# Optimization experiments

Hardware: AMD Instinct MI355X
Metric: run time of the kernel (lower is better)

The kernel has to match this reference:

```python
import jax, jax.numpy as jnp
import numpy as np
from jax import lax

B, S, H, T = 64, 512, 1024, 24


def setup_inputs() -> dict:
    key = jax.random.key(0)
    k1, k2, k3, k4, k5 = jax.random.split(key, 5)
    feats = jax.random.normal(k1, (B, S, H), dtype=jnp.float32)
    target = jax.random.randint(k2, (B, S), 0, T)  # tag ids (argmax of original one-hot target)
    # descending-sorted lengths -> prefix mask, matching the torch code's sorted-batch assumption
    lengths = jnp.sort(jax.random.randint(k3, (B,), S // 2, S + 1))[::-1]
    mask = jnp.arange(S)[None, :] < lengths[:, None]  # (B,S) bool
    # hidden2tag params (uniform init ~ nn.Linear default scale)
    bound = 1.0 / np.sqrt(H)
    W = jax.random.uniform(k4, (T, H), minval=-bound, maxval=bound, dtype=jnp.float32)
    b = jax.random.uniform(k5, (T,), minval=-bound, maxval=bound, dtype=jnp.float32)
    transition = jnp.zeros((T, T), dtype=jnp.float32)
    return {"feats": feats, "target": target, "mask": mask, "W": W, "b": b, "transition": transition}


def reference(feats, target, mask, W, b, transition):
    # emission scores: (B,S,T)
    emission = jnp.einsum("bsh,th->bst", feats, W) + b
    # gold path score
    sc = jnp.take_along_axis(emission, target[:, :, None], axis=2).squeeze(-1)  # (B,S)
    sc = sc.at[:, 1:].add(transition[target[:, :-1], target[:, 1:]])
    total_score = (sc * mask.astype(emission.dtype)).sum(axis=1)  # (B,)
    # forward algorithm (log-partition) as a scan over time
    p0 = emission[:, 0]  # (B,T)
    emis_t = jnp.swapaxes(emission[:, 1:], 0, 1)  # (S-1,B,T)
    mask_t = jnp.swapaxes(mask[:, 1:], 0, 1)      # (S-1,B)

    def step(p, xs):
        emit_i, m_i = xs
        # log_sum[b, prev, cur] = p[b, prev] + transition[prev, cur] + emit_i[b, cur]
        new_p = jax.nn.logsumexp(p[:, :, None] + transition[None, :, :] + emit_i[:, None, :], axis=1)
        return jnp.where(m_i[:, None], new_p, p), None

    p, _ = lax.scan(step, p0, (emis_t, mask_t))
    log_Z = jax.nn.logsumexp(p, axis=1)  # (B,)
    loss = -jnp.mean(total_score - log_Z)
    return loss, emission
```

## Files before the change

### kernel.cpp

```cpp
#include <hip/hip_runtime.h>
#include <cstdint>
#include <math.h>

#define B_ 64
#define S_ 512
#define H_ 1024
#define T_ 24
#define TP_ 32
#define NC_ 32
#define CL_ 16
#define KST_ 1040

typedef unsigned int u32;
typedef unsigned short u16;
typedef __attribute__((ext_vector_type(8))) short short8v;
typedef __attribute__((ext_vector_type(4))) float f32x4;
typedef __attribute__((ext_vector_type(4))) u32 uint4v;

__device__ __forceinline__ float rl_f32(float x, int sl) {
    return __uint_as_float(__builtin_amdgcn_readlane(__float_as_uint(x), sl));
}

__device__ __forceinline__ void split_pk(float f0, float f1, u32& hpk, u32& lpk) {
    const u32 u0 = __float_as_uint(f0), u1 = __float_as_uint(f1);
    const u32 t1 = u1 & 0xffff0000u;
    hpk = (u0 >> 16) | t1;
    const float fl0 = f0 - __uint_as_float(u0 & 0xffff0000u);
    const float fl1 = f1 - __uint_as_float(t1);
    lpk = (__float_as_uint(fl0) >> 16) | (__float_as_uint(fl1) & 0xffff0000u);
}

__global__ __launch_bounds__(256) void wcvt_kernel(const float* __restrict__ W,
                                                   u16* __restrict__ Wh,
                                                   u16* __restrict__ Wl,
                                                   float* __restrict__ out) {
    const int i = blockIdx.x * 256 + threadIdx.x;
    if (i == 0) out[0] = 0.f;
    const int t = i >> 10;
    const float f = (t < T_) ? W[i] : 0.f;
    const u32 u = __float_as_uint(f);
    const u32 rh = u + 0x7fffu + ((u >> 16) & 1u);
    const u16 hb = (u16)(rh >> 16);
    const float fh = __uint_as_float((u32)hb << 16);
    const float fl = f - fh;
    const u32 u2 = __float_as_uint(fl);
    const u32 rl2 = u2 + 0x7fffu + ((u2 >> 16) & 1u);
    Wh[i] = hb;
    Wl[i] = (u16)(rl2 >> 16);
}

__global__ __launch_bounds__(256, 4) void gemm_kernel(const float* __restrict__ feats,
                                                      const u16* __restrict__ Wh,
                                                      const u16* __restrict__ Wl,
                                                      const float* __restrict__ bias,
                                                      float* __restrict__ emission) {
    __shared__ f32x4 ldsP[2][64][2];
    const int tid  = threadIdx.x;
    const int lane = tid & 63;
    const int wv   = tid >> 6;
    const int mt_in = wv & 1;
    const int kh    = wv >> 1;
    const int r16  = lane & 15;
    const int g    = lane >> 4;
    const int mtile = blockIdx.x * 2 + mt_in;

    const long ko0 = (long)kh * 512 + g * 8;
    const float* ap  = feats + ((long)mtile * 16 + r16) * H_ + ko0;
    const u16* bh0p = Wh + r16 * H_ + ko0;
    const u16* bl0p = Wl + r16 * H_ + ko0;
    const u16* bh1p = Wh + (r16 + 16) * H_ + ko0;
    const u16* bl1p = Wl + (r16 + 16) * H_ + ko0;

    f32x4 acc0 = {0.f, 0.f, 0.f, 0.f};
    f32x4 acc1 = {0.f, 0.f, 0.f, 0.f};

    float4 A0[3], A1[3];
    short8v BH0[3], BL0[3], BH1[3], BL1[3];
#pragma unroll
    for (int p = 0; p < 3; ++p) {
        const int ko = p * 32;
        A0[p]  = *(const float4*)(ap + ko);
        A1[p]  = *(const float4*)(ap + ko + 4);
        BH0[p] = *(const short8v*)(bh0p + ko);
        BL0[p] = *(const short8v*)(bl0p + ko);
        BH1[p] = *(const short8v*)(bh1p + ko);
        BL1[p] = *(const short8v*)(bl1p + ko);
    }

#pragma unroll
    for (int kk = 0; kk < 16; ++kk) {
        const int sl = kk % 3;
        const float4 a0 = A0[sl];
        const float4 a1 = A1[sl];
        const short8v bh0 = BH0[sl];
        const short8v bl0 = BL0[sl];
        const short8v bh1 = BH1[sl];
        const short8v bl1 = BL1[sl];
        if (kk + 3 < 16) {
            const int ko = (kk + 3) * 32;
            A0[sl]  = *(const float4*)(ap + ko);
            A1[sl]  = *(const float4*)(ap + ko + 4);
            BH0[sl] = *(const short8v*)(bh0p + ko);
            BL0[sl] = *(const short8v*)(bl0p + ko);
            BH1[sl] = *(const short8v*)(bh1p + ko);
            BL1[sl] = *(const short8v*)(bl1p + ko);
        }

        u32 h0, l0, h1, l1, h2, l2, h3, l3;
        split_pk(a0.x, a0.y, h0, l0);
        split_pk(a0.z, a0.w, h1, l1);
        split_pk(a1.x, a1.y, h2, l2);
        split_pk(a1.z, a1.w, h3, l3);
        const uint4v hv = {h0, h1, h2, h3};
        const uint4v lv = {l0, l1, l2, l3};
        const short8v ah = __builtin_bit_cast(short8v, hv);
        const short8v al = __builtin_bit_cast(short8v, lv);

        acc0 = __builtin_amdgcn_mfma_f32_16x16x32_bf16(al, bh0, acc0, 0, 0, 0);
        acc0 = __builtin_amdgcn_mfma_f32_16x16x32_bf16(ah, bl0, acc0, 0, 0, 0);
        acc0 = __builtin_amdgcn_mfma_f32_16x16x32_bf16(ah, bh0, acc0, 0, 0, 0);
        acc1 = __builtin_amdgcn_mfma_f32_16x16x32_bf16(al, bh1, acc1, 0, 0, 0);
        acc1 = __builtin_amdgcn_mfma_f32_16x16x32_bf16(ah, bl1, acc1, 0, 0, 0);
        acc1 = __builtin_amdgcn_mfma_f32_16x16x32_bf16(ah, bh1, acc1, 0, 0, 0);
    }

    if (kh == 1) {
        ldsP[mt_in][lane][0] = acc0;
        ldsP[mt_in][lane][1] = acc1;
    }
    __syncthreads();
    if (kh == 0) {
        const f32x4 p0 = ldsP[mt_in][lane][0];
        const f32x4 p1 = ldsP[mt_in][lane][1];
#pragma unroll
        for (int r = 0; r < 4; ++r) {
            acc0[r] += p0[r];
            acc1[r] += p1[r];
        }
        const float b0 = bias[r16];
        const float b1 = (r16 + 16 < T_) ? bias[r16 + 16] : 0.f;
        float* op = emission + ((long)mtile * 16 + g * 4) * T_;
#pragma unroll
        for (int r = 0; r < 4; ++r) {
            op[r * T_ + r16] = acc0[r] + b0;
            if (r16 + 16 < T_) op[r * T_ + r16 + 16] = acc1[r] + b1;
        }
    }
}

__global__ __launch_bounds__(64, 1) void chunk_kernel(const float* __restrict__ emission,
                                                      const int* __restrict__ mask,
                                                      const float* __restrict__ trans,
                                                      float* __restrict__ wsK) {
    __shared__ u32 lds[2][2][16][18];
    const int bid = blockIdx.x;
    const int c_ = bid & (NC_ - 1);
    const int b  = bid >> 5;
    const int l  = threadIdx.x;
    const int cc = l & 15;
    const int q  = l >> 4;
    const int aq4 = (l & 48);

    const float* em = emission + (long)b * S_ * T_;
    const int* mk = mask + b * S_;

    int mc = 0;
#pragma unroll
    for (int k = 0; k < 8; ++k) mc += mk[l + k * 64];
#pragma unroll
    for (int off = 32; off; off >>= 1) mc += __shfl_xor(mc, off);
    const int len = __builtin_amdgcn_readfirstlane(mc);

    const int lo = 1 + c_ * CL_;
    const int hi = min(lo + CL_, S_);
    const int send = min(hi, len);

    short8v Ah[2], Al[2];
#pragma unroll
    for (int I = 0; I < 2; ++I) {
        const int j = 16 * I + cc;
        u32 hw[4], lw[4];
#pragma unroll
        for (int w = 0; w < 4; ++w) {
            const int t0 = 8 * q + 2 * w;
            const float v0 = (t0 < 24 && j < 24) ? __expf(trans[t0 * T_ + j]) : 0.f;
            const float v1 = (t0 + 1 < 24 && j < 24) ? __expf(trans[(t0 + 1) * T_ + j]) : 0.f;
            split_pk(v0, v1, hw[w], lw[w]);
        }
        const uint4v hv = {hw[0], hw[1], hw[2], hw[3]};
        const uint4v lv = {lw[0], lw[1], lw[2], lw[3]};
        Ah[I] = __builtin_bit_cast(short8v, hv);
        Al[I] = __builtin_bit_cast(short8v, lv);
    }

    f32x4 K[2][2];
#pragma unroll
    for (int I = 0; I < 2; ++I)
#pragma unroll
        for (int J = 0; J < 2; ++J)
#pragma unroll
            for (int r = 0; r < 4; ++r)
                K[I][J][r] = (16 * I + 4 * q + r == 16 * J + cc) ? 1.f : 0.f;

    u32 bh[2][4], bl[2][4];
#pragma unroll
    for (int J = 0; J < 2; ++J)
#pragma unroll
        for (int w = 0; w < 4; ++w) {
            const int k0 = 8 * q + 2 * w, col = 16 * J + cc;
            bh[J][w] = (k0 == col ? 0x3f80u : 0u) | (k0 + 1 == col ? 0x3f800000u : 0u);
            bl[J][w] = 0u;
        }

    const int xj = ((l & 31) < 24) ? (l & 31) : 0;
    float xr_[CL_];
#pragma unroll
    for (int k = 0; k < CL_; ++k) {
        const int s = lo + k;
        xr_[k] = em[((s < S_) ? s : 0) * T_ + xj];
    }

    float Ls = 0.f;
    const f32x4 z4 = {0.f, 0.f, 0.f, 0.f};

#pragma unroll
    for (int k = 0; k < CL_; ++k) {
        const int s = lo + k;
        if (s < send) {
            const uint4v bh0v = {bh[0][0], bh[0][1], bh[0][2], bh[0][3]};
            const uint4v bh1v = {bh[1][0], bh[1][1], bh[1][2], bh[1][3]};
            const uint4v bl0v = {bl[0][0], bl[0][1], bl[0][2], bl[0][3]};
            const uint4v bl1v = {bl[1][0], bl[1][1], bl[1][2], bl[1][3]};
            const short8v B0h = __builtin_bit_cast(short8v, bh0v);
            const short8v B1h = __builtin_bit_cast(short8v, bh1v);
            const short8v B0l = __builtin_bit_cast(short8v, bl0v);
            const short8v B1l = __builtin_bit_cast(short8v, bl1v);

            f32x4 acc[2][2];
#pragma unroll
            for (int I = 0; I < 2; ++I) {
                acc[I][0] = __builtin_amdgcn_mfma_f32_16x16x32_bf16(Ah[I], B0h, z4, 0, 0, 0);
                acc[I][0] = __builtin_amdgcn_mfma_f32_16x16x32_bf16(Ah[I], B0l, acc[I][0], 0, 0, 0);
                acc[I][0] = __builtin_amdgcn_mfma_f32_16x16x32_bf16(Al[I], B0h, acc[I][0], 0, 0, 0);
                acc[I][1] = __builtin_amdgcn_mfma_f32_16x16x32_bf16(Ah[I], B1h, z4, 0, 0, 0);
                acc[I][1] = __builtin_amdgcn_mfma_f32_16x16x32_bf16(Ah[I], B1l, acc[I][1], 0, 0, 0);
                acc[I][1] = __builtin_amdgcn_mfma_f32_16x16x32_bf16(Al[I], B1h, acc[I][1], 0, 0, 0);
            }

            const float X = __expf(xr_[k]);
            const int xi = __float_as_int(X);
            float xr0[4], xr1[4];
#pragma unroll
            for (int r = 0; r < 4; ++r) {
                xr0[r] = __int_as_float(__builtin_amdgcn_ds_bpermute(aq4 + 4 * r, xi));
                xr1[r] = __int_as_float(__builtin_amdgcn_ds_bpermute(aq4 + 64 + 4 * r, xi));
            }
#pragma unroll
            for (int J = 0; J < 2; ++J)
#pragma unroll
                for (int r = 0; r < 4; ++r) {
                    K[0][J][r] = acc[0][J][r] * xr0[r];
                    K[1][J][r] = acc[1][J][r] * xr1[r];
                }

            if (k == 7 || k == CL_ - 1) {
                float mx = K[0][0][0];
#pragma unroll
                for (int I = 0; I < 2; ++I)
#pragma unroll
                    for (int J = 0; J < 2; ++J)
#pragma unroll
                        for (int r = 0; r < 4; ++r) mx = fmaxf(mx, K[I][J][r]);
#pragma unroll
                for (int off = 32; off; off >>= 1) mx = fmaxf(mx, __shfl_xor(mx, off));
                const u32 ef = __float_as_uint(mx) & 0x7f800000u;
                const float inv = __uint_as_float(0x7f000000u - ef);
#pragma unroll
                for (int I = 0; I < 2; ++I)
#pragma unroll
                    for (int J = 0; J < 2; ++J)
#pragma unroll
                        for (int r = 0; r < 4; ++r) K[I][J][r] *= inv;
                Ls += (float)((int)(ef >> 23) - 127) * 0.6931471805599453f;
            }

            if (k < CL_ - 1) {
#pragma unroll
                for (int I = 0; I < 2; ++I)
#pragma unroll
                    for (int J = 0; J < 2; ++J)
#pragma unroll
                        for (int m = 0; m < 2; ++m) {
                            u32 h, lo_w;
                            split_pk(K[I][J][2 * m], K[I][J][2 * m + 1], h, lo_w);
                            const int p = 8 * I + 2 * q + m;
                            lds[0][J][p][cc] = h;
                            lds[1][J][p][cc] = lo_w;
                        }
#pragma unroll
                for (int J = 0; J < 2; ++J)
#pragma unroll
                    for (int w = 0; w < 4; ++w) {
                        bh[J][w] = lds[0][J][4 * q + w][cc];
                        bl[J][w] = lds[1][J][4 * q + w][cc];
                    }
            }
        }
    }

    float* outp = wsK + (long)(b * NC_ + c_) * KST_;
#pragma unroll
    for (int I = 0; I < 2; ++I)
#pragma unroll
        for (int J = 0; J < 2; ++J)
#pragma unroll
            for (int r = 0; r < 4; ++r)
                outp[(16 * I + 4 * q + r) * 32 + 16 * J + cc] = K[I][J][r];
    if (l == 0) outp[1024] = Ls;
}

#define ACC4(kv, t0)                                                           \
    s0 = fmaf(rl_f32(p, (t0) + 0), kv.x, s0);                                  \
    s1 = fmaf(rl_f32(p, (t0) + 1), kv.y, s1);                                  \
    s2 = fmaf(rl_f32(p, (t0) + 2), kv.z, s2);                                  \
    s3 = fmaf(rl_f32(p, (t0) + 3), kv.w, s3);

__global__ __launch_bounds__(64) void finalize_kernel(const float* __restrict__ emission,
                                                      const int* __restrict__ target,
                                                      const int* __restrict__ mask,
                                                      const float* __restrict__ trans,
                                                      const float* __restrict__ wsK,
                                                      float* __restrict__ out) {
    const int b = blockIdx.x;
    const int j = threadIdx.x;
    const int jj = j < 24 ? j : 23;
    const float* em = emission + (long)b * S_ * T_;
    const int* mk = mask + b * S_;

    float p = (j < 24) ? __expf(em[j]) : 0.f;
    float C = 0.f;

    for (int c = 0; c < NC_; ++c) {
        const float* base = wsK + (long)(b * NC_ + c) * KST_;
        C += base[1024];
        const float4* rp = (const float4*)(base + jj * 32);
        const float4 k0 = rp[0], k1 = rp[1], k2 = rp[2], k3 = rp[3], k4 = rp[4], k5 = rp[5];
        float s0 = 0.f, s1 = 0.f, s2 = 0.f, s3 = 0.f;
        ACC4(k0, 0) ACC4(k1, 4) ACC4(k2, 8) ACC4(k3, 12) ACC4(k4, 16) ACC4(k5, 20)
        p = (j < 24) ? ((s0 + s1) + (s2 + s3)) : 0.f;
        float mx = p;
#pragma unroll
        for (int off = 32; off; off >>= 1) mx = fmaxf(mx, __shfl_xor(mx, off));
        const u32 ef = __float_as_uint(mx) & 0x7f800000u;
        p *= __uint_as_float(0x7f000000u - ef);
        C += (float)((int)(ef >> 23) - 127) * 0.6931471805599453f;
    }

    float ex = p;
#pragma unroll
    for (int off = 32; off; off >>= 1) ex += __shfl_down(ex, off);

    float ssum = 0.f;
#pragma unroll
    for (int kk = 0; kk < S_ / 64; ++kk) {
        const int s = j + kk * 64;
        if (mk[s]) {
            const int tg = target[b * S_ + s];
            float v = em[s * T_ + tg];
            if (s > 0) v += trans[target[b * S_ + s - 1] * T_ + tg];
            ssum += v;
        }
    }
#pragma unroll
    for (int off = 32; off; off >>= 1) ssum += __shfl_down(ssum, off);

    if (j == 0) {
        const float logZ = C + __logf(ex);
        atomicAdd(out, (logZ - ssum) * (1.0f / B_));
    }
}

extern "C" void kernel_launch(void* const* d_in, const int* in_sizes, int n_in,
                              void* d_out, int out_size, void* d_ws, size_t ws_size,
                              hipStream_t stream) {
    const float* feats  = (const float*)d_in[0];
    const int*   target = (const int*)d_in[1];
    const int*   mask   = (const int*)d_in[2];
    const float* W      = (const float*)d_in[3];
    const float* bias   = (const float*)d_in[4];
    const float* trans  = (const float*)d_in[5];

    float* out = (float*)d_out;
    float* emission = out + 1;
    u16* Wh = (u16*)d_ws;
    u16* Wl = Wh + TP_ * H_;
    float* wsK = (float*)((char*)d_ws + 131072);

    wcvt_kernel<<<(TP_ * H_) / 256, 256, 0, stream>>>(W, Wh, Wl, out);
    gemm_kernel<<<1024, 256, 0, stream>>>(feats, Wh, Wl, bias, emission);
    chunk_kernel<<<B_ * NC_, 64, 0, stream>>>(emission, mask, trans, wsK);
    finalize_kernel<<<B_, 64, 0, stream>>>(emission, target, mask, trans, wsK, out);
}
```

Measured before the change: 259.0 us.

## Fuse finalize into chunk kernel via last-block-done atomic counter

Merges the finalize kernel into the chunk kernel. The last of the NC_ chunk blocks for each batch row, detected through a per-batch atomic counter that wcvt_kernel zeroes, performs the chunk-combine and loss reduction. This removes one kernel launch and its launch gap, and lets a batch's finalize start as soon as its chunks are done. The cost is threadfences and an atomic per block, plus a serial tail carried by whichever block finishes last.

Result: slower. 351.2 us (+35.6%).

```diff
diff --git a/kernel.cpp b/kernel.cpp
--- a/kernel.cpp
+++ b/kernel.cpp
@@ -33,9 +33,11 @@
 __global__ __launch_bounds__(256) void wcvt_kernel(const float* __restrict__ W,
                                                    u16* __restrict__ Wh,
                                                    u16* __restrict__ Wl,
-                                                   float* __restrict__ out) {
+                                                   float* __restrict__ out,
+                                                   int* __restrict__ cnt) {
     const int i = blockIdx.x * 256 + threadIdx.x;
     if (i == 0) out[0] = 0.f;
+    if (i < B_) cnt[i] = 0;
     const int t = i >> 10;
     const float f = (t < T_) ? W[i] : 0.f;
     const u32 u = __float_as_uint(f);
@@ -148,10 +150,13 @@
     }
 }
 
-__global__ __launch_bounds__(64, 1) void chunk_kernel(const float* __restrict__ emission,
-                                                      const int* __restrict__ mask,
-                                                      const float* __restrict__ trans,
-                                                      float* __restrict__ wsK) {
+__global__ __launch_bounds__(64, 1) void chunkfin_kernel(const float* __restrict__ emission,
+                                                         const int* __restrict__ target,
+                                                         const int* __restrict__ mask,
+                                                         const float* __restrict__ trans,
+                                                         float* __restrict__ wsK,
+                                                         int* __restrict__ cnt,
+                                                         float* __restrict__ out) {
     __shared__ u32 lds[2][2][16][18];
     const int bid = blockIdx.x;
     const int c_ = bid & (NC_ - 1);
@@ -317,26 +322,16 @@
             for (int r = 0; r < 4; ++r)
                 outp[(16 * I + 4 * q + r) * 32 + 16 * J + cc] = K[I][J][r];
     if (l == 0) outp[1024] = Ls;
-}
-
-#define ACC4(kv, t0)                                                           \
-    s0 = fmaf(rl_f32(p, (t0) + 0), kv.x, s0);                                  \
-    s1 = fmaf(rl_f32(p, (t0) + 1), kv.y, s1);                                  \
-    s2 = fmaf(rl_f32(p, (t0) + 2), kv.z, s2);                                  \
-    s3 = fmaf(rl_f32(p, (t0) + 3), kv.w, s3);
-
-__global__ __launch_bounds__(64) void finalize_kernel(const float* __restrict__ emission,
-                                                      const int* __restrict__ target,
-                                                      const int* __restrict__ mask,
-                                                      const float* __restrict__ trans,
-                                                      const float* __restrict__ wsK,
-                                                      float* __restrict__ out) {
-    const int b = blockIdx.x;
-    const int j = threadIdx.x;
+
+    __threadfence();
+    int myprev = 0;
+    if (l == 0) myprev = atomicAdd(cnt + b, 1);
+    myprev = __shfl(myprev, 0);
+    if (myprev != NC_ - 1) return;
+    __threadfence();
+
+    const int j = l;
     const int jj = j < 24 ? j : 23;
-    const float* em = emission + (long)b * S_ * T_;
-    const int* mk = mask + b * S_;
-
     float p = (j < 24) ? __expf(em[j]) : 0.f;
     float C = 0.f;
 
@@ -346,7 +341,13 @@
         const float4* rp = (const float4*)(base + jj * 32);
         const float4 k0 = rp[0], k1 = rp[1], k2 = rp[2], k3 = rp[3], k4 = rp[4], k5 = rp[5];
         float s0 = 0.f, s1 = 0.f, s2 = 0.f, s3 = 0.f;
+#define ACC4(kv, t0)                                                           \
+        s0 = fmaf(rl_f32(p, (t0) + 0), kv.x, s0);                              \
+        s1 = fmaf(rl_f32(p, (t0) + 1), kv.y, s1);                              \
+        s2 = fmaf(rl_f32(p, (t0) + 2), kv.z, s2);                              \
+        s3 = fmaf(rl_f32(p, (t0) + 3), kv.w, s3);
         ACC4(k0, 0) ACC4(k1, 4) ACC4(k2, 8) ACC4(k3, 12) ACC4(k4, 16) ACC4(k5, 20)
+#undef ACC4
         p = (j < 24) ? ((s0 + s1) + (s2 + s3)) : 0.f;
         float mx = p;
 #pragma unroll
@@ -395,9 +396,9 @@
     u16* Wh = (u16*)d_ws;
     u16* Wl = Wh + TP_ * H_;
     float* wsK = (float*)((char*)d_ws + 131072);
-
-    wcvt_kernel<<<(TP_ * H_) / 256, 256, 0, stream>>>(W, Wh, Wl, out);
+    int* cnt = (int*)((char*)d_ws + 131072 + (size_t)B_ * NC_ * KST_ * 4);
+
+    wcvt_kernel<<<(TP_ * H_) / 256, 256, 0, stream>>>(W, Wh, Wl, out, cnt);
     gemm_kernel<<<1024, 256, 0, stream>>>(feats, Wh, Wl, bias, emission);
-    chunk_kernel<<<B_ * NC_, 64, 0, stream>>>(emission, mask, trans, wsK);
-    finalize_kernel<<<B_, 64, 0, stream>>>(emission, target, mask, trans, wsK, out);
-}
+    chunkfin_kernel<<<B_ * NC_, 64, 0, stream>>>(emission, target, mask, trans, wsK, cnt, out);
+}
```
